# Kernel tuning notes

Hardware: AMD Instinct MI355X
Metric: run time of the kernel (lower is better)

The kernel has to match this reference:

```python
import jax, jax.numpy as jnp
import numpy as np

EPS = 1e-12  # F.normalize clamp_min eps


def setup_inputs() -> dict:
    key = jax.random.key(0)
    k1, k2, k3, k4 = jax.random.split(key, 4)
    E, A, D, S = 1000000, 100000, 128, 1024
    return {
        "edge_weights": jax.random.uniform(k1, (E,), dtype=jnp.float32),
        "s_indices": jax.random.randint(k2, (E,), 0, S, dtype=jnp.int32),
        "a_indices": jax.random.randint(k3, (E,), 0, A, dtype=jnp.int32),
        "agent_features": jax.random.normal(k4, (A, D), dtype=jnp.float32),
        "num_s": S,
    }


def reference(edge_weights, s_indices, a_indices, agent_features, num_s):
    # Per-edge gathered agent features: [E, D]
    feats_e = agent_features[a_indices]
    ones = jnp.ones_like(edge_weights)
    counts = jax.ops.segment_sum(ones, s_indices, num_segments=num_s)  # [S]
    safe_counts = jnp.maximum(counts, 1.0)

    # Per-source mean feature: [S, D]
    sum_feats = jax.ops.segment_sum(feats_e, s_indices, num_segments=num_s)
    mean_feats = sum_feats / safe_counts[:, None]

    # L2-normalize (eps-clamped norm, matching F.normalize)
    feats_norm = feats_e / jnp.maximum(
        jnp.linalg.norm(feats_e, axis=1, keepdims=True), EPS)
    mean_norm = mean_feats / jnp.maximum(
        jnp.linalg.norm(mean_feats, axis=1, keepdims=True), EPS)

    # Cosine similarity of each edge's agent features to its source mean: [E]
    sims = jnp.sum(feats_norm * mean_norm[s_indices], axis=1)

    # Per-source mean weight, per-edge variance, similarity-weighted variance
    mean_w = jax.ops.segment_sum(edge_weights, s_indices, num_segments=num_s) / safe_counts
    var = (edge_weights - mean_w[s_indices]) ** 2
    wv = sims * var

    # Per-source mean of weighted variance; sources with <=1 edge contribute 0
    seg_mean_wv = jax.ops.segment_sum(wv, s_indices, num_segments=num_s) / safe_counts
    valid = counts > 1.0
    total = jnp.sum(jnp.where(valid, seg_mean_wv, 0.0))
    return total / num_s
```

## Files before the change

### kernel.cpp

```cpp
#include <hip/hip_runtime.h>
#include <math.h>

#define EPS 1e-12f

static constexpr int S_FIXED = 1024;
static constexpr int D_DIM   = 128;
static constexpr int NBLK    = 256;

typedef float floatx2 __attribute__((ext_vector_type(2)));

#if defined(__has_builtin)
#if __has_builtin(__builtin_amdgcn_cvt_pk_fp8_f32) && __has_builtin(__builtin_amdgcn_cvt_pk_f32_fp8)
#define USE_HW_FP8 1
#endif
#endif

template <bool HI>
static __device__ __forceinline__ unsigned enc_pair(float a, float b, unsigned old) {
#ifdef USE_HW_FP8
    return (unsigned)__builtin_amdgcn_cvt_pk_fp8_f32(a, b, (int)old, HI);
#else
    auto enc1 = [](float x) -> unsigned {
        unsigned u   = __float_as_uint(x);
        unsigned s   = (u >> 24) & 0x80u;
        unsigned mag = u & 0x7fffffffu;
        unsigned byte;
        if (mag >= 0x3C800000u) {
            unsigned rb = mag + 0x7ffffu + ((mag >> 20) & 1u);
            byte = s | (((rb >> 20) - 960u) & 0x7fu);
        } else {
            float t = __uint_as_float(mag) * 512.0f;
            unsigned m = (unsigned)(int)rintf(t);
            byte = s | m;
        }
        return byte;
    };
    unsigned v = enc1(a) | (enc1(b) << 8);
    return HI ? ((old & 0x0000ffffu) | (v << 16)) : ((old & 0xffff0000u) | v);
#endif
}

template <bool HI>
static __device__ __forceinline__ floatx2 dec_pair(unsigned v) {
#ifdef USE_HW_FP8
    return __builtin_amdgcn_cvt_pk_f32_fp8(v, HI);
#else
    auto dec1 = [](unsigned b) -> float {
        unsigned t = (b & 0x7fu) << 20;
        float a = __uint_as_float(t + 0x3C800000u);
        float r = (t < (1u << 23)) ? (a - 0.015625f) : (0.5f * a);
        return (b & 0x80u) ? -r : r;
    };
    unsigned h = HI ? (v >> 16) : (v & 0xffffu);
    floatx2 o;
    o.x = dec1(h & 0xffu);
    o.y = dec1((h >> 8) & 0xffu);
    return o;
#endif
}

static __device__ __forceinline__ unsigned pack_wr(float w, float r) {
    _Float16 hw = (_Float16)w, hr = (_Float16)r;
    unsigned short bw, br;
    __builtin_memcpy(&bw, &hw, 2);
    __builtin_memcpy(&br, &hr, 2);
    return (unsigned)bw | ((unsigned)br << 16);
}
static __device__ __forceinline__ float2 unpack_wr(unsigned u) {
    unsigned short bw = (unsigned short)(u & 0xffffu), br = (unsigned short)(u >> 16);
    _Float16 hw, hr;
    __builtin_memcpy(&hw, &bw, 2);
    __builtin_memcpy(&hr, &br, 2);
    return make_float2((float)hw, (float)hr);
}

__global__ __launch_bounds__(256) void normhist_kernel(const float* __restrict__ feats,
                                                       unsigned char* __restrict__ g8,
                                                       float* __restrict__ r_tab, int A,
                                                       const int* __restrict__ s_idx,
                                                       int* __restrict__ counts2d,
                                                       int E, int chunk, int ncb,
                                                       float* __restrict__ out) {
    if (blockIdx.x == 0 && threadIdx.x == 0) out[0] = 0.0f;
    if (blockIdx.x < (unsigned)ncb) {
        const int row = blockIdx.x * 16 + (threadIdx.x >> 4);
        const int sl  = threadIdx.x & 15;
        if (row >= A) return;
        const float4* fp = reinterpret_cast<const float4*>(feats + (size_t)row * D_DIM + sl * 8);
        const float4 v0 = fp[0], v1 = fp[1];
        float ss = v0.x*v0.x + v0.y*v0.y + v0.z*v0.z + v0.w*v0.w
                 + v1.x*v1.x + v1.y*v1.y + v1.z*v1.z + v1.w*v1.w;
#pragma unroll
        for (int o = 1; o < 16; o <<= 1) ss += __shfl_xor(ss, o);
        const float nrm = sqrtf(ss);
        const float inv = 1.0f / fmaxf(nrm, EPS);
        unsigned lo = enc_pair<false>(v0.x*inv, v0.y*inv, 0u);
        lo = enc_pair<true>(v0.z*inv, v0.w*inv, lo);
        unsigned hi = enc_pair<false>(v1.x*inv, v1.y*inv, 0u);
        hi = enc_pair<true>(v1.z*inv, v1.w*inv, hi);
        *reinterpret_cast<uint2*>(g8 + (size_t)row * D_DIM + sl * 8) = make_uint2(lo, hi);
        if (sl == 0) r_tab[row] = nrm;
    } else {
        __shared__ int h[S_FIXED];
        for (int i = threadIdx.x; i < S_FIXED; i += 256) h[i] = 0;
        __syncthreads();
        const int b  = blockIdx.x - ncb;
        const int lo = b * chunk;
        const int hi = min(E, lo + chunk);
        for (int i = lo + threadIdx.x; i < hi; i += 256)
            atomicAdd(&h[s_idx[i]], 1);
        __syncthreads();
        for (int i = threadIdx.x; i < S_FIXED; i += 256)
            counts2d[b * S_FIXED + i] = h[i];
    }
}

__global__ __launch_bounds__(256) void scan_blocks_kernel(int* __restrict__ counts2d,
                                                          int* __restrict__ counts) {
    const int wv = threadIdx.x >> 6, lane = threadIdx.x & 63;
    const int bin = blockIdx.x * 4 + wv;
    int running = 0;
#pragma unroll
    for (int b0 = 0; b0 < NBLK; b0 += 64) {
        const int idx = (b0 + lane) * S_FIXED + bin;
        const int c = counts2d[idx];
        int inc = c;
#pragma unroll
        for (int o = 1; o < 64; o <<= 1) {
            int t = __shfl_up(inc, o);
            if (lane >= o) inc += t;
        }
        counts2d[idx] = running + inc - c;
        running += __shfl(inc, 63);
    }
    if (lane == 0) counts[bin] = running;
}

__global__ __launch_bounds__(256) void scatter3_kernel(const int* __restrict__ s_idx,
                                                       const int* __restrict__ a_idx,
                                                       const float* __restrict__ w,
                                                       const float* __restrict__ r_tab,
                                                       const int* __restrict__ counts2d,
                                                       const int* __restrict__ counts,
                                                       uint2* __restrict__ bin8,
                                                       int E, int chunk) {
    __shared__ int cur[S_FIXED];
    __shared__ int tsum[256];
    const int b = blockIdx.x;
    const int t = threadIdx.x;

    int c[4]; int sum = 0;
#pragma unroll
    for (int i = 0; i < 4; ++i) { c[i] = counts[t * 4 + i]; sum += c[i]; }
    tsum[t] = sum;
    __syncthreads();
    for (int off = 1; off < 256; off <<= 1) {
        int v = (t >= off) ? tsum[t - off] : 0;
        __syncthreads();
        tsum[t] += v;
        __syncthreads();
    }
    int base = tsum[t] - sum;
#pragma unroll
    for (int i = 0; i < 4; ++i) {
        const int bi = t * 4 + i;
        cur[bi] = base + counts2d[b * S_FIXED + bi];
        base += c[i];
    }
    __syncthreads();

    const int lo = b * chunk;
    const int hi = min(E, lo + chunk);
    for (int i = lo + threadIdx.x; i < hi; i += 256) {
        const int s   = s_idx[i];
        const int a   = a_idx[i];
        const int pos = atomicAdd(&cur[s], 1);
        bin8[pos] = make_uint2((unsigned)a, pack_wr(w[i], r_tab[a]));
    }
}

__global__ __launch_bounds__(512) void partial_finish_kernel(
    const unsigned char* __restrict__ g8,
    const int*           __restrict__ counts,
    const uint2*         __restrict__ bin8,
    const int*           __restrict__ num_s_ptr,
    float*               __restrict__ out,
    int A)
{
    const int s     = blockIdx.x;
    const int cnt   = counts[s];
    const int wave  = threadIdx.x >> 6;
    const int lane  = threadIdx.x & 63;
    const int egrp  = lane >> 5;
    const int sl    = lane & 31;

    const int start = counts[S_FIXED + s];
    const int end   = start + cnt;

    floatx2 acc[4][2];
#pragma unroll
    for (int v = 0; v < 4; ++v)
#pragma unroll
        for (int q = 0; q < 2; ++q) acc[v][q] = (floatx2)(0.0f);
    float accW = 0.0f;

    auto body = [&](uint2 rec, bool valid) {
        const unsigned aj = min(rec.x, (unsigned)(A - 1));
        const float2 wr = unpack_wr(rec.y);
        const float wj  = valid ? wr.x : 0.0f;
        const float rj  = valid ? wr.y : 0.0f;
        const float cuv = valid ? 1.0f : 0.0f;
        accW += wj;
        const unsigned gu = *reinterpret_cast<const unsigned*>(g8 + (size_t)aj * D_DIM + sl * 4);
        floatx2 f[2];
        f[0] = dec_pair<false>(gu);
        f[1] = dec_pair<true>(gu);
        const floatx2 cr  = (floatx2)(rj);
        const floatx2 cu  = (floatx2)(cuv);
        const floatx2 cw  = (floatx2)(wj);
        const floatx2 cw2 = (floatx2)(wj * wj);
#pragma unroll
        for (int q = 0; q < 2; ++q) {
            acc[0][q] = __builtin_elementwise_fma(cr,  f[q], acc[0][q]);
            acc[1][q] = __builtin_elementwise_fma(cu,  f[q], acc[1][q]);
            acc[2][q] = __builtin_elementwise_fma(cw,  f[q], acc[2][q]);
            acc[3][q] = __builtin_elementwise_fma(cw2, f[q], acc[3][q]);
        }
    };

    for (int base = start + wave * 64; base < end; base += 512) {
        const int rem = min(64, end - base);
        if (rem == 64) {
#pragma unroll
            for (int j = 0; j < 32; ++j)
                body(bin8[base + 2 * j + egrp], true);
        } else {
            const int jfull = rem >> 1;
            for (int j = 0; j < jfull; ++j)
                body(bin8[base + 2 * j + egrp], true);
            if (rem & 1) {
                const int e = (rem & ~1) + egrp;
                body(bin8[base + e], e < rem);
            }
        }
    }

#pragma unroll
    for (int v = 0; v < 4; ++v)
#pragma unroll
        for (int q = 0; q < 2; ++q) {
            acc[v][q].x += __shfl_xor(acc[v][q].x, 32);
            acc[v][q].y += __shfl_xor(acc[v][q].y, 32);
        }
#pragma unroll
    for (int o = 32; o > 0; o >>= 1) accW += __shfl_xor(accW, o);

    __shared__ float red[8][4 * D_DIM];
    __shared__ float redW[8];
    if (lane < 32) {
#pragma unroll
        for (int v = 0; v < 4; ++v)
#pragma unroll
            for (int q = 0; q < 2; ++q) {
                red[wave][v * D_DIM + sl * 4 + 2 * q]     = acc[v][q].x;
                red[wave][v * D_DIM + sl * 4 + 2 * q + 1] = acc[v][q].y;
            }
    }
    if (lane == 0) redW[wave] = accW * (1.0f / 32.0f);
    __syncthreads();

    if (wave == 0) {
        float2 V[4];
#pragma unroll
        for (int v = 0; v < 4; ++v) {
            const int d = v * D_DIM + lane * 2;
            float vx = 0.f, vy = 0.f;
#pragma unroll
            for (int k = 0; k < 8; ++k) { vx += red[k][d]; vy += red[k][d + 1]; }
            V[v] = make_float2(vx, vy);
        }
        const float safe     = (float)max(cnt, 1);
        const float inv_safe = 1.0f / safe;

        const float mx = V[0].x * inv_safe, my = V[0].y * inv_safe;
        float ss = mx * mx + my * my;
        float s0 = V[1].x * mx + V[1].y * my;
        float s1 = V[2].x * mx + V[2].y * my;
        float s2 = V[3].x * mx + V[3].y * my;
#pragma unroll
        for (int o = 32; o > 0; o >>= 1) {
            ss += __shfl_xor(ss, o);
            s0 += __shfl_xor(s0, o);
            s1 += __shfl_xor(s1, o);
            s2 += __shfl_xor(s2, o);
        }
        if (lane == 0 && cnt > 1) {
            float sumW = 0.f;
#pragma unroll
            for (int k = 0; k < 8; ++k) sumW += redW[k];
            const float mw = sumW * inv_safe;
            const float mn = fmaxf(sqrtf(ss), EPS);
            const float contrib = (s2 - 2.0f * mw * s1 + mw * mw * s0) / mn * inv_safe
                                  / (float)(*num_s_ptr);
            atomicAdd(out, contrib);
        }
    }
}

__global__ __launch_bounds__(1024) void scan_bins_kernel(int* __restrict__ counts) {
    __shared__ int sh[S_FIXED];
    const int t = threadIdx.x;
    const int c = counts[t];
    sh[t] = c;
    __syncthreads();
    for (int off = 1; off < S_FIXED; off <<= 1) {
        int v = (t >= off) ? sh[t - off] : 0;
        __syncthreads();
        sh[t] += v;
        __syncthreads();
    }
    counts[S_FIXED + t] = sh[t] - c;
}

extern "C" void kernel_launch(void* const* d_in, const int* in_sizes, int n_in,
                              void* d_out, int out_size, void* d_ws, size_t ws_size,
                              hipStream_t stream) {
    const float* edge_w  = (const float*)d_in[0];
    const int*   s_idx   = (const int*)d_in[1];
    const int*   a_idx   = (const int*)d_in[2];
    const float* feats   = (const float*)d_in[3];
    const int*   num_s_p = (const int*)d_in[4];

    const int E = in_sizes[0];
    const int A = in_sizes[3] / D_DIM;

    float* out = (float*)d_out;

    char* p = (char*)d_ws;
    uint2*         bin8     = (uint2*)p;         p += (size_t)E * 8;
    int*           counts2d = (int*)p;           p += (size_t)NBLK * S_FIXED * 4;
    int*           counts   = (int*)p;           p += 2 * S_FIXED * 4;
    float*         r_tab    = (float*)p;         p += (size_t)A * 4;
    unsigned char* g8       = (unsigned char*)p; p += (size_t)A * D_DIM;

    const int chunk = (E + NBLK - 1) / NBLK;
    const int ncb   = (A + 15) / 16;

    normhist_kernel<<<ncb + NBLK, 256, 0, stream>>>(feats, g8, r_tab, A,
                                                    s_idx, counts2d, E, chunk, ncb, out);
    scan_blocks_kernel<<<S_FIXED / 4, 256, 0, stream>>>(counts2d, counts);
    scan_bins_kernel<<<1, 1024, 0, stream>>>(counts);
    scatter3_kernel<<<NBLK, 256, 0, stream>>>(s_idx, a_idx, edge_w, r_tab, counts2d,
                                              counts, bin8, E, chunk);
    partial_finish_kernel<<<S_FIXED, 512, 0, stream>>>(g8, counts, bin8, num_s_p, out, A);
}
```

Before: 80.59 us.

## Slice fp8 feature table by dimension quarter and map slices to XCDs

The normalized fp8 feature table is split into four 32-dimension slices, each stored contiguously. The per-source reduction is split into four blocks per source, one per slice, and the block index is mapped so each slice lands on a pair of XCDs. The intent is that each XCD's L2 holds only its slice of the 12.8MB table and gather hits improve. Partial dot products are combined with atomics into a small per-source buffer, and a new single-block final kernel reduces them. The bin-offset scan is folded into the scatter kernel, which removes the separate scan launch. In exchange, the binned edge list is read four times, and the change adds one more launch plus per-source atomics.

New measurement: 78.63 us. -2.4%, faster.

```diff
diff --git a/kernel.cpp b/kernel.cpp
--- a/kernel.cpp
+++ b/kernel.cpp
@@ -6,6 +6,7 @@
 static constexpr int S_FIXED = 1024;
 static constexpr int D_DIM   = 128;
 static constexpr int NBLK    = 256;
+static constexpr int NSLICE  = 4;
 
 typedef float floatx2 __attribute__((ext_vector_type(2)));
 
@@ -75,7 +76,7 @@
 }
 
 __global__ __launch_bounds__(256) void normhist_kernel(const float* __restrict__ feats,
-                                                       unsigned char* __restrict__ g8,
+                                                       unsigned char* __restrict__ g8s,
                                                        float* __restrict__ r_tab, int A,
                                                        const int* __restrict__ s_idx,
                                                        int* __restrict__ counts2d,
@@ -98,7 +99,9 @@
         lo = enc_pair<true>(v0.z*inv, v0.w*inv, lo);
         unsigned hi = enc_pair<false>(v1.x*inv, v1.y*inv, 0u);
         hi = enc_pair<true>(v1.z*inv, v1.w*inv, hi);
-        *reinterpret_cast<uint2*>(g8 + (size_t)row * D_DIM + sl * 8) = make_uint2(lo, hi);
+        const int q = sl >> 2;
+        *reinterpret_cast<uint2*>(g8s + ((size_t)q * A + row) * 32 + (sl & 3) * 8)
+            = make_uint2(lo, hi);
         if (sl == 0) r_tab[row] = nrm;
     } else {
         __shared__ int h[S_FIXED];
@@ -141,7 +144,8 @@
                                                        const float* __restrict__ w,
                                                        const float* __restrict__ r_tab,
                                                        const int* __restrict__ counts2d,
-                                                       const int* __restrict__ counts,
+                                                       int* __restrict__ counts,
+                                                       float* __restrict__ sdots,
                                                        uint2* __restrict__ bin8,
                                                        int E, int chunk) {
     __shared__ int cur[S_FIXED];
@@ -165,8 +169,11 @@
     for (int i = 0; i < 4; ++i) {
         const int bi = t * 4 + i;
         cur[bi] = base + counts2d[b * S_FIXED + bi];
+        if (b == 0) counts[S_FIXED + bi] = base;
         base += c[i];
     }
+    if (b == 0)
+        for (int i = t; i < S_FIXED * 8; i += 256) sdots[i] = 0.0f;
     __syncthreads();
 
     const int lo = b * chunk;
@@ -179,29 +186,33 @@
     }
 }
 
-__global__ __launch_bounds__(512) void partial_finish_kernel(
-    const unsigned char* __restrict__ g8,
+__global__ __launch_bounds__(256) void partial_slice_kernel(
+    const unsigned char* __restrict__ g8s,
     const int*           __restrict__ counts,
     const uint2*         __restrict__ bin8,
-    const int*           __restrict__ num_s_ptr,
-    float*               __restrict__ out,
+    float*               __restrict__ sdots,
     int A)
 {
-    const int s     = blockIdx.x;
+    const int b   = blockIdx.x;
+    const int xcd = b & 7;
+    const int q   = xcd >> 1;
+    const int s   = ((b >> 3) << 1) | (xcd & 1);
+
     const int cnt   = counts[s];
+    const int start = counts[S_FIXED + s];
+    const int end   = start + cnt;
     const int wave  = threadIdx.x >> 6;
     const int lane  = threadIdx.x & 63;
-    const int egrp  = lane >> 5;
-    const int sl    = lane & 31;
-
-    const int start = counts[S_FIXED + s];
-    const int end   = start + cnt;
+    const int eg    = lane >> 3;
+    const int dl    = lane & 7;
+
+    const unsigned char* gq = g8s + (size_t)q * A * 32;
 
     floatx2 acc[4][2];
 #pragma unroll
     for (int v = 0; v < 4; ++v)
 #pragma unroll
-        for (int q = 0; q < 2; ++q) acc[v][q] = (floatx2)(0.0f);
+        for (int k = 0; k < 2; ++k) acc[v][k] = (floatx2)(0.0f);
     float accW = 0.0f;
 
     auto body = [&](uint2 rec, bool valid) {
@@ -211,7 +222,7 @@
         const float rj  = valid ? wr.y : 0.0f;
         const float cuv = valid ? 1.0f : 0.0f;
         accW += wj;
-        const unsigned gu = *reinterpret_cast<const unsigned*>(g8 + (size_t)aj * D_DIM + sl * 4);
+        const unsigned gu = *reinterpret_cast<const unsigned*>(gq + (size_t)aj * 32 + dl * 4);
         floatx2 f[2];
         f[0] = dec_pair<false>(gu);
         f[1] = dec_pair<true>(gu);
@@ -220,26 +231,26 @@
         const floatx2 cw  = (floatx2)(wj);
         const floatx2 cw2 = (floatx2)(wj * wj);
 #pragma unroll
-        for (int q = 0; q < 2; ++q) {
-            acc[0][q] = __builtin_elementwise_fma(cr,  f[q], acc[0][q]);
-            acc[1][q] = __builtin_elementwise_fma(cu,  f[q], acc[1][q]);
-            acc[2][q] = __builtin_elementwise_fma(cw,  f[q], acc[2][q]);
-            acc[3][q] = __builtin_elementwise_fma(cw2, f[q], acc[3][q]);
+        for (int k = 0; k < 2; ++k) {
+            acc[0][k] = __builtin_elementwise_fma(cr,  f[k], acc[0][k]);
+            acc[1][k] = __builtin_elementwise_fma(cu,  f[k], acc[1][k]);
+            acc[2][k] = __builtin_elementwise_fma(cw,  f[k], acc[2][k]);
+            acc[3][k] = __builtin_elementwise_fma(cw2, f[k], acc[3][k]);
         }
     };
 
-    for (int base = start + wave * 64; base < end; base += 512) {
+    for (int base = start + wave * 64; base < end; base += 256) {
         const int rem = min(64, end - base);
         if (rem == 64) {
 #pragma unroll
-            for (int j = 0; j < 32; ++j)
-                body(bin8[base + 2 * j + egrp], true);
+            for (int j = 0; j < 8; ++j)
+                body(bin8[base + 8 * j + eg], true);
         } else {
-            const int jfull = rem >> 1;
-            for (int j = 0; j < jfull; ++j)
-                body(bin8[base + 2 * j + egrp], true);
-            if (rem & 1) {
-                const int e = (rem & ~1) + egrp;
+            const int jf = rem >> 3;
+            for (int j = 0; j < jf; ++j)
+                body(bin8[base + 8 * j + eg], true);
+            if (rem & 7) {
+                const int e = (rem & ~7) + eg;
                 body(bin8[base + e], e < rem);
             }
         }
@@ -248,78 +259,95 @@
 #pragma unroll
     for (int v = 0; v < 4; ++v)
 #pragma unroll
-        for (int q = 0; q < 2; ++q) {
-            acc[v][q].x += __shfl_xor(acc[v][q].x, 32);
-            acc[v][q].y += __shfl_xor(acc[v][q].y, 32);
+        for (int k = 0; k < 2; ++k) {
+#pragma unroll
+            for (int o = 8; o <= 32; o <<= 1) {
+                acc[v][k].x += __shfl_xor(acc[v][k].x, o);
+                acc[v][k].y += __shfl_xor(acc[v][k].y, o);
+            }
         }
 #pragma unroll
     for (int o = 32; o > 0; o >>= 1) accW += __shfl_xor(accW, o);
 
-    __shared__ float red[8][4 * D_DIM];
-    __shared__ float redW[8];
-    if (lane < 32) {
+    __shared__ float red[4][4 * 32];
+    __shared__ float redW[4];
+    if (lane < 8) {
 #pragma unroll
         for (int v = 0; v < 4; ++v)
 #pragma unroll
-            for (int q = 0; q < 2; ++q) {
-                red[wave][v * D_DIM + sl * 4 + 2 * q]     = acc[v][q].x;
-                red[wave][v * D_DIM + sl * 4 + 2 * q + 1] = acc[v][q].y;
+            for (int k = 0; k < 2; ++k) {
+                red[wave][v * 32 + dl * 4 + 2 * k]     = acc[v][k].x;
+                red[wave][v * 32 + dl * 4 + 2 * k + 1] = acc[v][k].y;
             }
     }
-    if (lane == 0) redW[wave] = accW * (1.0f / 32.0f);
+    if (lane == 0) redW[wave] = accW;
     __syncthreads();
 
-    if (wave == 0) {
-        float2 V[4];
-#pragma unroll
-        for (int v = 0; v < 4; ++v) {
-            const int d = v * D_DIM + lane * 2;
-            float vx = 0.f, vy = 0.f;
-#pragma unroll
-            for (int k = 0; k < 8; ++k) { vx += red[k][d]; vy += red[k][d + 1]; }
-            V[v] = make_float2(vx, vy);
-        }
-        const float safe     = (float)max(cnt, 1);
-        const float inv_safe = 1.0f / safe;
-
-        const float mx = V[0].x * inv_safe, my = V[0].y * inv_safe;
-        float ss = mx * mx + my * my;
-        float s0 = V[1].x * mx + V[1].y * my;
-        float s1 = V[2].x * mx + V[2].y * my;
-        float s2 = V[3].x * mx + V[3].y * my;
-#pragma unroll
-        for (int o = 32; o > 0; o >>= 1) {
-            ss += __shfl_xor(ss, o);
-            s0 += __shfl_xor(s0, o);
-            s1 += __shfl_xor(s1, o);
-            s2 += __shfl_xor(s2, o);
-        }
-        if (lane == 0 && cnt > 1) {
-            float sumW = 0.f;
-#pragma unroll
-            for (int k = 0; k < 8; ++k) sumW += redW[k];
-            const float mw = sumW * inv_safe;
-            const float mn = fmaxf(sqrtf(ss), EPS);
-            const float contrib = (s2 - 2.0f * mw * s1 + mw * mw * s0) / mn * inv_safe
-                                  / (float)(*num_s_ptr);
-            atomicAdd(out, contrib);
-        }
-    }
-}
-
-__global__ __launch_bounds__(1024) void scan_bins_kernel(int* __restrict__ counts) {
-    __shared__ int sh[S_FIXED];
-    const int t = threadIdx.x;
-    const int c = counts[t];
-    sh[t] = c;
+    if (wave == 0 && lane < 32) {
+        const int d = lane;
+        float V0 = 0.f, V1 = 0.f, V2 = 0.f, V3 = 0.f;
+#pragma unroll
+        for (int k = 0; k < 4; ++k) {
+            V0 += red[k][0 * 32 + d];
+            V1 += red[k][1 * 32 + d];
+            V2 += red[k][2 * 32 + d];
+            V3 += red[k][3 * 32 + d];
+        }
+        const float inv_safe = 1.0f / (float)max(cnt, 1);
+        const float m = V0 * inv_safe;
+        float pss = m * m;
+        float ps0 = V1 * m;
+        float ps1 = V2 * m;
+        float ps2 = V3 * m;
+#pragma unroll
+        for (int o = 16; o > 0; o >>= 1) {
+            pss += __shfl_xor(pss, o);
+            ps0 += __shfl_xor(ps0, o);
+            ps1 += __shfl_xor(ps1, o);
+            ps2 += __shfl_xor(ps2, o);
+        }
+        if (lane == 0) {
+            atomicAdd(&sdots[s * 8 + 0], pss);
+            atomicAdd(&sdots[s * 8 + 1], ps0);
+            atomicAdd(&sdots[s * 8 + 2], ps1);
+            atomicAdd(&sdots[s * 8 + 3], ps2);
+            atomicAdd(&sdots[s * 8 + 4], redW[0] + redW[1] + redW[2] + redW[3]);
+        }
+    }
+}
+
+__global__ __launch_bounds__(1024) void final_kernel(const float* __restrict__ sdots,
+                                                     const int* __restrict__ counts,
+                                                     const int* __restrict__ num_s_ptr,
+                                                     float* __restrict__ out) {
+    const int s    = threadIdx.x;
+    const int wv   = s >> 6;
+    const int lane = s & 63;
+    const int cnt  = counts[s];
+    float contrib = 0.0f;
+    if (cnt > 1) {
+        const float ss   = sdots[s * 8 + 0];
+        const float s0   = sdots[s * 8 + 1];
+        const float s1   = sdots[s * 8 + 2];
+        const float s2   = sdots[s * 8 + 3];
+        const float sumW = sdots[s * 8 + 4] * (1.0f / 32.0f);
+        const float inv_safe = 1.0f / (float)cnt;
+        const float mw = sumW * inv_safe;
+        const float mn = fmaxf(sqrtf(ss), EPS);
+        contrib = (s2 - 2.0f * mw * s1 + mw * mw * s0) / mn * inv_safe
+                  / (float)(*num_s_ptr);
+    }
+#pragma unroll
+    for (int o = 32; o > 0; o >>= 1) contrib += __shfl_xor(contrib, o);
+    __shared__ float bl[16];
+    if (lane == 0) bl[wv] = contrib;
     __syncthreads();
-    for (int off = 1; off < S_FIXED; off <<= 1) {
-        int v = (t >= off) ? sh[t - off] : 0;
-        __syncthreads();
-        sh[t] += v;
-        __syncthreads();
-    }
-    counts[S_FIXED + t] = sh[t] - c;
+    if (s == 0) {
+        float t = 0.0f;
+#pragma unroll
+        for (int i = 0; i < 16; ++i) t += bl[i];
+        out[0] = t;
+    }
 }
 
 extern "C" void kernel_launch(void* const* d_in, const int* in_sizes, int n_in,
@@ -340,17 +368,18 @@
     uint2*         bin8     = (uint2*)p;         p += (size_t)E * 8;
     int*           counts2d = (int*)p;           p += (size_t)NBLK * S_FIXED * 4;
     int*           counts   = (int*)p;           p += 2 * S_FIXED * 4;
+    float*         sdots    = (float*)p;         p += S_FIXED * 8 * 4;
     float*         r_tab    = (float*)p;         p += (size_t)A * 4;
-    unsigned char* g8       = (unsigned char*)p; p += (size_t)A * D_DIM;
+    unsigned char* g8s      = (unsigned char*)p; p += (size_t)NSLICE * A * 32;
 
     const int chunk = (E + NBLK - 1) / NBLK;
     const int ncb   = (A + 15) / 16;
 
-    normhist_kernel<<<ncb + NBLK, 256, 0, stream>>>(feats, g8, r_tab, A,
+    normhist_kernel<<<ncb + NBLK, 256, 0, stream>>>(feats, g8s, r_tab, A,
                                                     s_idx, counts2d, E, chunk, ncb, out);
     scan_blocks_kernel<<<S_FIXED / 4, 256, 0, stream>>>(counts2d, counts);
-    scan_bins_kernel<<<1, 1024, 0, stream>>>(counts);
     scatter3_kernel<<<NBLK, 256, 0, stream>>>(s_idx, a_idx, edge_w, r_tab, counts2d,
-                                              counts, bin8, E, chunk);
-    partial_finish_kernel<<<S_FIXED, 512, 0, stream>>>(g8, counts, bin8, num_s_p, out, A);
-}
+                                              counts, sdots, bin8, E, chunk);
+    partial_slice_kernel<<<S_FIXED * NSLICE, 256, 0, stream>>>(g8s, counts, bin8, sdots, A);
+    final_kernel<<<1, 1024, 0, stream>>>(sdots, counts, num_s_p, out);
+}
```

## Drop scan_bins launch and move norm lookup from scatter to finish kernel

Applied to the files above, without the earlier changes.

Removes the separate single-block bin-prefix-scan kernel. Block 0 of the scatter kernel now writes the bin start offsets it already computes. The per-agent norm is stored as fp16 in a compact table and read in the finish kernel, rather than gathered during scatter and packed with the weight. The weight is now stored as full fp32 in the edge record. This takes the random r_tab gather out of scatter and saves one launch, at the cost of an extra random 2-byte gather per edge in the finish kernel.

Measured after the change: 100.8 us. 1.25x slower.

```diff
diff --git a/kernel.cpp b/kernel.cpp
--- a/kernel.cpp
+++ b/kernel.cpp
@@ -59,24 +59,9 @@
 #endif
 }
 
-static __device__ __forceinline__ unsigned pack_wr(float w, float r) {
-    _Float16 hw = (_Float16)w, hr = (_Float16)r;
-    unsigned short bw, br;
-    __builtin_memcpy(&bw, &hw, 2);
-    __builtin_memcpy(&br, &hr, 2);
-    return (unsigned)bw | ((unsigned)br << 16);
-}
-static __device__ __forceinline__ float2 unpack_wr(unsigned u) {
-    unsigned short bw = (unsigned short)(u & 0xffffu), br = (unsigned short)(u >> 16);
-    _Float16 hw, hr;
-    __builtin_memcpy(&hw, &bw, 2);
-    __builtin_memcpy(&hr, &br, 2);
-    return make_float2((float)hw, (float)hr);
-}
-
 __global__ __launch_bounds__(256) void normhist_kernel(const float* __restrict__ feats,
                                                        unsigned char* __restrict__ g8,
-                                                       float* __restrict__ r_tab, int A,
+                                                       _Float16* __restrict__ r16, int A,
                                                        const int* __restrict__ s_idx,
                                                        int* __restrict__ counts2d,
                                                        int E, int chunk, int ncb,
@@ -99,7 +84,7 @@
         unsigned hi = enc_pair<false>(v1.x*inv, v1.y*inv, 0u);
         hi = enc_pair<true>(v1.z*inv, v1.w*inv, hi);
         *reinterpret_cast<uint2*>(g8 + (size_t)row * D_DIM + sl * 8) = make_uint2(lo, hi);
-        if (sl == 0) r_tab[row] = nrm;
+        if (sl == 0) r16[row] = (_Float16)nrm;
     } else {
         __shared__ int h[S_FIXED];
         for (int i = threadIdx.x; i < S_FIXED; i += 256) h[i] = 0;
@@ -139,9 +124,8 @@
 __global__ __launch_bounds__(256) void scatter3_kernel(const int* __restrict__ s_idx,
                                                        const int* __restrict__ a_idx,
                                                        const float* __restrict__ w,
-                                                       const float* __restrict__ r_tab,
                                                        const int* __restrict__ counts2d,
-                                                       const int* __restrict__ counts,
+                                                       int* __restrict__ counts,
                                                        uint2* __restrict__ bin8,
                                                        int E, int chunk) {
     __shared__ int cur[S_FIXED];
@@ -165,6 +149,7 @@
     for (int i = 0; i < 4; ++i) {
         const int bi = t * 4 + i;
         cur[bi] = base + counts2d[b * S_FIXED + bi];
+        if (b == 0) counts[S_FIXED + bi] = base;
         base += c[i];
     }
     __syncthreads();
@@ -173,14 +158,14 @@
     const int hi = min(E, lo + chunk);
     for (int i = lo + threadIdx.x; i < hi; i += 256) {
         const int s   = s_idx[i];
-        const int a   = a_idx[i];
         const int pos = atomicAdd(&cur[s], 1);
-        bin8[pos] = make_uint2((unsigned)a, pack_wr(w[i], r_tab[a]));
+        bin8[pos] = make_uint2((unsigned)a_idx[i], __float_as_uint(w[i]));
     }
 }
 
 __global__ __launch_bounds__(512) void partial_finish_kernel(
     const unsigned char* __restrict__ g8,
+    const _Float16*      __restrict__ r16,
     const int*           __restrict__ counts,
     const uint2*         __restrict__ bin8,
     const int*           __restrict__ num_s_ptr,
@@ -206,9 +191,8 @@
 
     auto body = [&](uint2 rec, bool valid) {
         const unsigned aj = min(rec.x, (unsigned)(A - 1));
-        const float2 wr = unpack_wr(rec.y);
-        const float wj  = valid ? wr.x : 0.0f;
-        const float rj  = valid ? wr.y : 0.0f;
+        const float wj  = valid ? __uint_as_float(rec.y) : 0.0f;
+        const float rj  = valid ? (float)r16[aj] : 0.0f;
         const float cuv = valid ? 1.0f : 0.0f;
         accW += wj;
         const unsigned gu = *reinterpret_cast<const unsigned*>(g8 + (size_t)aj * D_DIM + sl * 4);
@@ -307,21 +291,6 @@
     }
 }
 
-__global__ __launch_bounds__(1024) void scan_bins_kernel(int* __restrict__ counts) {
-    __shared__ int sh[S_FIXED];
-    const int t = threadIdx.x;
-    const int c = counts[t];
-    sh[t] = c;
-    __syncthreads();
-    for (int off = 1; off < S_FIXED; off <<= 1) {
-        int v = (t >= off) ? sh[t - off] : 0;
-        __syncthreads();
-        sh[t] += v;
-        __syncthreads();
-    }
-    counts[S_FIXED + t] = sh[t] - c;
-}
-
 extern "C" void kernel_launch(void* const* d_in, const int* in_sizes, int n_in,
                               void* d_out, int out_size, void* d_ws, size_t ws_size,
                               hipStream_t stream) {
@@ -340,17 +309,17 @@
     uint2*         bin8     = (uint2*)p;         p += (size_t)E * 8;
     int*           counts2d = (int*)p;           p += (size_t)NBLK * S_FIXED * 4;
     int*           counts   = (int*)p;           p += 2 * S_FIXED * 4;
-    float*         r_tab    = (float*)p;         p += (size_t)A * 4;
+    _Float16*      r16      = (_Float16*)p;      p += (size_t)A * 2;
     unsigned char* g8       = (unsigned char*)p; p += (size_t)A * D_DIM;
 
     const int chunk = (E + NBLK - 1) / NBLK;
     const int ncb   = (A + 15) / 16;
 
-    normhist_kernel<<<ncb + NBLK, 256, 0, stream>>>(feats, g8, r_tab, A,
+    normhist_kernel<<<ncb + NBLK, 256, 0, stream>>>(feats, g8, r16, A,
                                                     s_idx, counts2d, E, chunk, ncb, out);
     scan_blocks_kernel<<<S_FIXED / 4, 256, 0, stream>>>(counts2d, counts);
-    scan_bins_kernel<<<1, 1024, 0, stream>>>(counts);
-    scatter3_kernel<<<NBLK, 256, 0, stream>>>(s_idx, a_idx, edge_w, r_tab, counts2d,
+    scatter3_kernel<<<NBLK, 256, 0, stream>>>(s_idx, a_idx, edge_w, counts2d,
                                               counts, bin8, E, chunk);
-    partial_finish_kernel<<<S_FIXED, 512, 0, stream>>>(g8, counts, bin8, num_s_p, out, A);
-}
+    partial_finish_kernel<<<S_FIXED, 512, 0, stream>>>(g8, r16, counts, bin8,
+                                                       num_s_p, out, A);
+}
```
